# Kernel optimization log

Measured on AMD Instinct MI355X. Metric: run time of the kernel, lower is better.

Reference implementation:

```python
import jax, jax.numpy as jnp
import numpy as np

D = 768
N_HEADS = 24
WH, WW = 7, 7
N = WH * WW  # 49 tokens per window
NW = 64      # windows per image
B_ = 2048    # num_windows * batch
HEAD_DIM = D // N_HEADS
SCALE = HEAD_DIM ** -0.5


def _relative_position_index():
    # Same construction as the torch module (numpy, static).
    coords = np.stack(np.meshgrid(np.arange(WH), np.arange(WW), indexing='ij'))  # (2,Wh,Ww)
    cf = coords.reshape(2, -1)                                  # (2, N)
    rel = cf[:, :, None] - cf[:, None, :]                       # (2, N, N)
    rel = rel.transpose(1, 2, 0)                                # (N, N, 2)
    rel[:, :, 0] += WH - 1
    rel[:, :, 1] += WW - 1
    rel[:, :, 0] *= 2 * WW - 1
    return rel.sum(-1)                                          # (N, N) int

REL_IDX = jnp.asarray(_relative_position_index())


def setup_inputs() -> dict:
    key = jax.random.key(0)
    ks = jax.random.split(key, 7)
    x = jax.random.normal(ks[0], (B_, N, D), dtype=jnp.float32)
    # 0 / -100 shifted-window style mask (finite stand-in for -inf)
    mask = jnp.where(jax.random.uniform(ks[1], (NW, N, N)) < 0.1, -100.0, 0.0).astype(jnp.float32)
    qkv_w = jax.random.normal(ks[2], (D, 3 * D), dtype=jnp.float32) * (D ** -0.5)
    qkv_b = jnp.zeros((3 * D,), dtype=jnp.float32)
    proj_w = jax.random.normal(ks[3], (D, D), dtype=jnp.float32) * (D ** -0.5)
    proj_b = jnp.zeros((D,), dtype=jnp.float32)
    bias_table = jax.random.normal(ks[4], ((2 * WH - 1) * (2 * WW - 1), N_HEADS), dtype=jnp.float32) * 0.02
    return {"x": x, "mask": mask, "qkv_w": qkv_w, "qkv_b": qkv_b,
            "proj_w": proj_w, "proj_b": proj_b, "bias_table": bias_table}


def reference(x, mask, qkv_w, qkv_b, proj_w, proj_b, bias_table):
    B, n, d = x.shape
    qkv = x @ qkv_w + qkv_b                                     # (B_, n, 3d)
    q, k, v = jnp.split(qkv, 3, axis=-1)
    # (B_, n, H, hd) -> (B_, H, n, hd)
    q = q.reshape(B, n, N_HEADS, HEAD_DIM).transpose(0, 2, 1, 3)
    k = k.reshape(B, n, N_HEADS, HEAD_DIM).transpose(0, 2, 1, 3)
    v = v.reshape(B, n, N_HEADS, HEAD_DIM).transpose(0, 2, 1, 3)
    logits = jnp.einsum('bhid,bhjd->bhij', q, k) * SCALE        # (B_, H, n, n)
    rel_bias = bias_table[REL_IDX]                              # (n, n, H)
    logits = logits + rel_bias.transpose(2, 0, 1)[None]         # add (1, H, n, n)
    nW = mask.shape[0]
    logits = logits.reshape(B // nW, nW, N_HEADS, n, n) + mask[None, :, None]
    logits = logits.reshape(B, N_HEADS, n, n)
    attn = jax.nn.softmax(logits, axis=-1)
    out = jnp.einsum('bhij,bhjd->bhid', attn, v)                # (B_, H, n, hd)
    out = out.transpose(0, 2, 1, 3).reshape(B, n, d)
    return out @ proj_w + proj_b
```

## Files before the change

### kernel.cpp

```cpp
#include <hip/hip_runtime.h>

typedef __attribute__((ext_vector_type(8))) short short8;
typedef __attribute__((ext_vector_type(4))) float floatx4;
typedef __attribute__((ext_vector_type(4))) unsigned short ushort4v;

#define SCALE_F 0.17677669529663687f

__device__ __forceinline__ unsigned short f2bf(float f) {
  union { float f; unsigned u; } v; v.f = f;
  unsigned u = v.u;
  u += 0x7fffu + ((u >> 16) & 1u);
  return (unsigned short)(u >> 16);
}

__device__ __forceinline__ void gld_lds16(const void* g, void* l) {
  __builtin_amdgcn_global_load_lds((const __attribute__((address_space(1))) void*)g,
                                   (__attribute__((address_space(3))) void*)l, 16, 0, 0);
}

__global__ __launch_bounds__(256)
void cvt_bf16_k(const float* __restrict__ src, unsigned short* __restrict__ dst, long n) {
  long i = ((long)blockIdx.x * 256 + threadIdx.x) * 8;
  if (i >= n) return;
  floatx4 a0 = *(const floatx4*)(src + i);
  floatx4 a1 = *(const floatx4*)(src + i + 4);
  short8 v;
  #pragma unroll
  for (int j = 0; j < 4; ++j) { v[j] = (short)f2bf(a0[j]); v[4 + j] = (short)f2bf(a1[j]); }
  *(short8*)(dst + i) = v;
}

__global__ __launch_bounds__(256)
void transcvt_k(const float* __restrict__ W, unsigned short* __restrict__ Wt, int K, int N) {
  __shared__ float t[64][65];
  const int n0 = blockIdx.x * 64, k0 = blockIdx.y * 64;
  const int tx = threadIdx.x & 15, ty = threadIdx.x >> 4;
  #pragma unroll
  for (int r = 0; r < 4; ++r) {
    floatx4 v = *(const floatx4*)&W[(long)(k0 + ty + r * 16) * N + n0 + tx * 4];
    #pragma unroll
    for (int j = 0; j < 4; ++j) t[ty + r * 16][tx * 4 + j] = v[j];
  }
  __syncthreads();
  #pragma unroll
  for (int r = 0; r < 4; ++r) {
    ushort4v o;
    #pragma unroll
    for (int j = 0; j < 4; ++j) o[j] = f2bf(t[tx * 4 + j][ty + r * 16]);
    *(ushort4v*)&Wt[(long)(n0 + ty + r * 16) * K + k0 + tx * 4] = o;
  }
}

template<bool OUT_F32>
__global__ __launch_bounds__(512, 2)
void gemm256(const unsigned short* __restrict__ A, const unsigned short* __restrict__ Bt,
             const float* __restrict__ bias, void* __restrict__ Cp,
             int M, int N, int K, int ntN) {
  __shared__ __align__(16) unsigned short sm[2][2][256 * 64];
  (void)M;
  const int tid  = threadIdx.x;
  const int wave = tid >> 6, lane = tid & 63;
  const int quad = lane >> 4, l15 = lane & 15;
  const int wm = wave >> 2, wn = wave & 3;
  const int xorw = (l15 & 7) << 3;

  const int nwg = gridDim.x;
  const int wg  = (blockIdx.x & 7) * (nwg >> 3) + (blockIdx.x >> 3);
  const int tileN = wg % ntN, tileM = wg / ntN;
  const int NT = K >> 6;

  const int srow = tid >> 3;
  const int sg   = (tid & 7) ^ (srow & 7);
  const unsigned short* Asrc = A  + (long)(tileM * 256 + srow) * K + sg * 8;
  const unsigned short* Bsrc = Bt + (long)(tileN * 256 + srow) * K + sg * 8;

#define STG(bufi, isB, h, tt) do {                                              \
    const unsigned short* _s = (isB) ? Bsrc : Asrc;                             \
    unsigned short* _d = &sm[bufi][isB][((h) * 128 + wave * 8) * 64];           \
    gld_lds16(_s + (long)((h) * 128) * K + (tt) * 64, _d);                      \
    gld_lds16(_s + (long)((h) * 128 + 64) * K + (tt) * 64, _d + 64 * 64);       \
  } while (0)

#define RD_A(mt, kk) (*(const short8*)&sm[cur][0][(wm * 128 + (mt) * 16 + l15) * 64 + (((kk) * 32 + quad * 8) ^ xorw)])
#define RD_B(nt, kk) (*(const short8*)&sm[cur][1][(wn * 64  + (nt) * 16 + l15) * 64 + (((kk) * 32 + quad * 8) ^ xorw)])

  short8 aF[4][2], bF[4][2];
  floatx4 acc[8][4] = {};

  STG(0, 1, 0, 0);
  STG(0, 0, 0, 0);
  STG(0, 0, 1, 0);
  STG(0, 1, 1, 0);
  if (NT > 1) {
    STG(1, 1, 0, 1);
    STG(1, 0, 0, 1);
    asm volatile("s_waitcnt vmcnt(4)" ::: "memory");
  } else {
    asm volatile("s_waitcnt vmcnt(0)" ::: "memory");
  }
  __builtin_amdgcn_s_barrier();

  for (int t = 0; t < NT; ++t) {
    const int cur = t & 1;
    #pragma unroll
    for (int mt = 0; mt < 4; ++mt)
      #pragma unroll
      for (int kk = 0; kk < 2; ++kk) aF[mt][kk] = RD_A(mt, kk);
    #pragma unroll
    for (int nt = 0; nt < 2; ++nt)
      #pragma unroll
      for (int kk = 0; kk < 2; ++kk) bF[nt][kk] = RD_B(nt, kk);
    if (t + 1 < NT) STG(cur ^ 1, 0, 1, t + 1);
    __builtin_amdgcn_s_barrier();
    asm volatile("s_waitcnt lgkmcnt(0)" ::: "memory");
    __builtin_amdgcn_s_setprio(1);
    #pragma unroll
    for (int mt = 0; mt < 4; ++mt)
      #pragma unroll
      for (int nt = 0; nt < 2; ++nt)
        #pragma unroll
        for (int kk = 0; kk < 2; ++kk)
          acc[mt][nt] = __builtin_amdgcn_mfma_f32_16x16x32_bf16(aF[mt][kk], bF[nt][kk], acc[mt][nt], 0, 0, 0);
    __builtin_amdgcn_s_setprio(0);
    __builtin_amdgcn_s_barrier();

    #pragma unroll
    for (int nt = 2; nt < 4; ++nt)
      #pragma unroll
      for (int kk = 0; kk < 2; ++kk) bF[nt][kk] = RD_B(nt, kk);
    if (t + 1 < NT) STG(cur ^ 1, 1, 1, t + 1);
    __builtin_amdgcn_s_barrier();
    asm volatile("s_waitcnt lgkmcnt(0)" ::: "memory");
    __builtin_amdgcn_s_setprio(1);
    #pragma unroll
    for (int mt = 0; mt < 4; ++mt)
      #pragma unroll
      for (int nt = 2; nt < 4; ++nt)
        #pragma unroll
        for (int kk = 0; kk < 2; ++kk)
          acc[mt][nt] = __builtin_amdgcn_mfma_f32_16x16x32_bf16(aF[mt][kk], bF[nt][kk], acc[mt][nt], 0, 0, 0);
    __builtin_amdgcn_s_setprio(0);
    __builtin_amdgcn_s_barrier();

    #pragma unroll
    for (int mt = 0; mt < 4; ++mt)
      #pragma unroll
      for (int kk = 0; kk < 2; ++kk) aF[mt][kk] = RD_A(mt + 4, kk);
    if (t + 2 < NT) STG(cur, 1, 0, t + 2);
    __builtin_amdgcn_s_barrier();
    asm volatile("s_waitcnt lgkmcnt(0)" ::: "memory");
    __builtin_amdgcn_s_setprio(1);
    #pragma unroll
    for (int mt = 0; mt < 4; ++mt)
      #pragma unroll
      for (int nt = 2; nt < 4; ++nt)
        #pragma unroll
        for (int kk = 0; kk < 2; ++kk)
          acc[mt + 4][nt] = __builtin_amdgcn_mfma_f32_16x16x32_bf16(aF[mt][kk], bF[nt][kk], acc[mt + 4][nt], 0, 0, 0);
    __builtin_amdgcn_s_setprio(0);
    __builtin_amdgcn_s_barrier();

    if (t + 2 < NT) STG(cur, 0, 0, t + 2);
    __builtin_amdgcn_s_setprio(1);
    #pragma unroll
    for (int mt = 0; mt < 4; ++mt)
      #pragma unroll
      for (int nt = 0; nt < 2; ++nt)
        #pragma unroll
        for (int kk = 0; kk < 2; ++kk)
          acc[mt + 4][nt] = __builtin_amdgcn_mfma_f32_16x16x32_bf16(aF[mt][kk], bF[nt][kk], acc[mt + 4][nt], 0, 0, 0);
    __builtin_amdgcn_s_setprio(0);
    if (t + 2 < NT)      { asm volatile("s_waitcnt vmcnt(4)" ::: "memory"); }
    else if (t + 1 < NT) { asm volatile("s_waitcnt vmcnt(0)" ::: "memory"); }
    __builtin_amdgcn_s_barrier();
  }
#undef STG
#undef RD_A
#undef RD_B

  float bv[4];
  #pragma unroll
  for (int nt = 0; nt < 4; ++nt) bv[nt] = bias[tileN * 256 + wn * 64 + nt * 16 + l15];
  #pragma unroll
  for (int mt = 0; mt < 8; ++mt)
    #pragma unroll
    for (int nt = 0; nt < 4; ++nt)
      #pragma unroll
      for (int r = 0; r < 4; ++r) {
        long rg = (long)tileM * 256 + wm * 128 + mt * 16 + quad * 4 + r;
        long cg = (long)tileN * 256 + wn * 64 + nt * 16 + l15;
        float val = acc[mt][nt][r] + bv[nt];
        if (OUT_F32) ((float*)Cp)[rg * (long)N + cg] = val;
        else         ((unsigned short*)Cp)[rg * (long)N + cg] = f2bf(val);
      }
}

__global__ __launch_bounds__(256)
void attn_k(const unsigned short* __restrict__ qkv, const float* __restrict__ mask,
            const float* __restrict__ bias_table, unsigned short* __restrict__ attn_out) {
  __shared__ __align__(16) unsigned short P[4][64][72];
  const int wave = threadIdx.x >> 6, lane = threadIdx.x & 63;
  const int quad = lane >> 4, l15 = lane & 15;
  const int flat = blockIdx.x * 4 + wave;
  const int b = flat / 24, h = flat % 24;

  const unsigned short* qbase = qkv + (long)b * 49 * 2304 + h * 32;
  const unsigned short* kbase = qbase + 768;
  const unsigned short* vbase = qbase + 1536;

  short8 qF[4], kF[4];
  #pragma unroll
  for (int mt = 0; mt < 4; ++mt) {
    int m = mt * 16 + l15; int me = m < 49 ? m : 48;
    qF[mt] = *(const short8*)(qbase + (long)me * 2304 + quad * 8);
  }
  #pragma unroll
  for (int nt = 0; nt < 4; ++nt) {
    int n = nt * 16 + l15; int ne = n < 49 ? n : 48;
    kF[nt] = *(const short8*)(kbase + (long)ne * 2304 + quad * 8);
  }

  floatx4 sc[4][4] = {};
  #pragma unroll
  for (int mt = 0; mt < 4; ++mt)
    #pragma unroll
    for (int nt = 0; nt < 4; ++nt)
      sc[mt][nt] = __builtin_amdgcn_mfma_f32_16x16x32_bf16(qF[mt], kF[nt], sc[mt][nt], 0, 0, 0);

  const int w = b & 63;
  const float* mrow = mask + (long)w * 49 * 49;
  #pragma unroll
  for (int mt = 0; mt < 4; ++mt)
    #pragma unroll
    for (int r = 0; r < 4; ++r) {
      int i = mt * 16 + quad * 4 + r;
      bool iv = i < 49;
      int ri = i / 7, ci = i % 7;
      float vals[4];
      float vmax = -1e30f;
      #pragma unroll
      for (int nt = 0; nt < 4; ++nt) {
        int j = nt * 16 + l15;
        float v = -1e30f;
        if (iv && j < 49) {
          int rj = j / 7, cj = j % 7;
          int idx = (ri - rj + 6) * 13 + (ci - cj + 6);
          v = sc[mt][nt][r] * SCALE_F + bias_table[idx * 24 + h] + mrow[i * 49 + j];
        }
        vals[nt] = v;
        vmax = fmaxf(vmax, v);
      }
      #pragma unroll
      for (int d = 1; d < 16; d <<= 1) vmax = fmaxf(vmax, __shfl_xor(vmax, d));
      float sum = 0.f;
      #pragma unroll
      for (int nt = 0; nt < 4; ++nt) { float e = __expf(vals[nt] - vmax); vals[nt] = e; sum += e; }
      #pragma unroll
      for (int d = 1; d < 16; d <<= 1) sum += __shfl_xor(sum, d);
      float inv = 1.0f / sum;
      #pragma unroll
      for (int nt = 0; nt < 4; ++nt)
        P[wave][i][nt * 16 + l15] = f2bf(vals[nt] * inv);
    }
  __syncthreads();

  floatx4 o[4][2] = {};
  #pragma unroll
  for (int kt = 0; kt < 2; ++kt) {
    short8 pF[4];
    #pragma unroll
    for (int mt = 0; mt < 4; ++mt)
      pF[mt] = *(const short8*)&P[wave][mt * 16 + l15][kt * 32 + quad * 8];
    short8 vF[2];
    #pragma unroll
    for (int nt = 0; nt < 2; ++nt) {
      short8 t;
      #pragma unroll
      for (int jj = 0; jj < 8; ++jj) {
        int j = kt * 32 + quad * 8 + jj; int je = j < 49 ? j : 48;
        t[jj] = (short)vbase[(long)je * 2304 + nt * 16 + l15];
      }
      vF[nt] = t;
    }
    #pragma unroll
    for (int mt = 0; mt < 4; ++mt)
      #pragma unroll
      for (int nt = 0; nt < 2; ++nt)
        o[mt][nt] = __builtin_amdgcn_mfma_f32_16x16x32_bf16(pF[mt], vF[nt], o[mt][nt], 0, 0, 0);
  }

  unsigned short* obase = attn_out + (long)b * 49 * 768 + h * 32;
  #pragma unroll
  for (int mt = 0; mt < 4; ++mt)
    #pragma unroll
    for (int nt = 0; nt < 2; ++nt)
      #pragma unroll
      for (int r = 0; r < 4; ++r) {
        int i = mt * 16 + quad * 4 + r;
        if (i < 49) obase[(long)i * 768 + nt * 16 + l15] = f2bf(o[mt][nt][r]);
      }
}

extern "C" void kernel_launch(void* const* d_in, const int* in_sizes, int n_in,
                              void* d_out, int out_size, void* d_ws, size_t ws_size,
                              hipStream_t stream) {
  const float* x          = (const float*)d_in[0];
  const float* mask       = (const float*)d_in[1];
  const float* qkv_w      = (const float*)d_in[2];
  const float* qkv_b      = (const float*)d_in[3];
  const float* proj_w     = (const float*)d_in[4];
  const float* proj_b     = (const float*)d_in[5];
  const float* bias_table = (const float*)d_in[6];

  unsigned short* xb      = (unsigned short*)d_out;
  unsigned short* qkv_wt  = (unsigned short*)d_out + (size_t)100352 * 768;
  unsigned short* qkv     = (unsigned short*)d_ws;
  unsigned short* attn    = qkv + (size_t)100352 * 2304;
  unsigned short* proj_wt = qkv;
  float* out = (float*)d_out;

  const long nx = (long)100352 * 768;
  cvt_bf16_k<<<(nx / 8 + 255) / 256, 256, 0, stream>>>(x, xb, nx);
  transcvt_k<<<dim3(36, 12), 256, 0, stream>>>(qkv_w, qkv_wt, 768, 2304);
  gemm256<false><<<dim3(3528), 512, 0, stream>>>(xb, qkv_wt, qkv_b, qkv, 100352, 2304, 768, 9);
  attn_k<<<12288, 256, 0, stream>>>(qkv, mask, bias_table, attn);
  transcvt_k<<<dim3(12, 12), 256, 0, stream>>>(proj_w, proj_wt, 768, 768);
  gemm256<true><<<dim3(1176), 512, 0, stream>>>(attn, proj_wt, proj_b, out, 100352, 768, 768, 3);
}
```

Measured before the change: 1.278 ms.

## Write V transposed per window from QKV GEMM epilogue for vectorized attention loads

The QKV GEMM epilogue now splits its output: Q and K go to a compact 1536-wide buffer, and V is written transposed into a per-window [b][channel][64] layout. The attention kernel then reads V fragments with single 16-byte loads instead of eight scalar strided gathers. MFMA sections are also bracketed with raised wave priority. The cost is scattered 2-byte stores in the GEMM epilogue and a larger padded V buffer placed in the output region.

```diff
diff --git a/kernel.cpp b/kernel.cpp
--- a/kernel.cpp
+++ b/kernel.cpp
@@ -55,9 +55,10 @@
 __global__ __launch_bounds__(512, 2)
 void gemm256(const unsigned short* __restrict__ A, const unsigned short* __restrict__ Bt,
              const float* __restrict__ bias, void* __restrict__ Cp,
-             int M, int N, int K, int ntN) {
+             unsigned short* __restrict__ Vt, int ldC, int vSplit,
+             int N, int K, int ntN) {
   __shared__ __align__(16) unsigned short sm[2][2][256 * 64];
-  (void)M;
+  (void)N;
   const int tid  = threadIdx.x;
   const int wave = tid >> 6, lane = tid & 63;
   const int quad = lane >> 4, l15 = lane & 15;
@@ -181,51 +182,71 @@
   float bv[4];
   #pragma unroll
   for (int nt = 0; nt < 4; ++nt) bv[nt] = bias[tileN * 256 + wn * 64 + nt * 16 + l15];
-  #pragma unroll
-  for (int mt = 0; mt < 8; ++mt)
-    #pragma unroll
-    for (int nt = 0; nt < 4; ++nt)
+  const int cg0 = tileN * 256 + wn * 64;
+
+  if (cg0 >= vSplit) {
+    #pragma unroll
+    for (int mt = 0; mt < 8; ++mt)
       #pragma unroll
       for (int r = 0; r < 4; ++r) {
-        long rg = (long)tileM * 256 + wm * 128 + mt * 16 + quad * 4 + r;
-        long cg = (long)tileN * 256 + wn * 64 + nt * 16 + l15;
-        float val = acc[mt][nt][r] + bv[nt];
-        if (OUT_F32) ((float*)Cp)[rg * (long)N + cg] = val;
-        else         ((unsigned short*)Cp)[rg * (long)N + cg] = f2bf(val);
+        int rg = tileM * 256 + wm * 128 + mt * 16 + quad * 4 + r;
+        int b = rg / 49, i = rg - b * 49;
+        #pragma unroll
+        for (int nt = 0; nt < 4; ++nt) {
+          int c = cg0 + nt * 16 + l15 - vSplit;
+          Vt[((long)b * 768 + c) * 64 + i] = f2bf(acc[mt][nt][r] + bv[nt]);
+        }
       }
+  } else {
+    #pragma unroll
+    for (int mt = 0; mt < 8; ++mt)
+      #pragma unroll
+      for (int nt = 0; nt < 4; ++nt)
+        #pragma unroll
+        for (int r = 0; r < 4; ++r) {
+          long rg = (long)tileM * 256 + wm * 128 + mt * 16 + quad * 4 + r;
+          long cg = cg0 + nt * 16 + l15;
+          float val = acc[mt][nt][r] + bv[nt];
+          if (OUT_F32) ((float*)Cp)[rg * (long)ldC + cg] = val;
+          else         ((unsigned short*)Cp)[rg * (long)ldC + cg] = f2bf(val);
+        }
+  }
 }
 
 __global__ __launch_bounds__(256)
-void attn_k(const unsigned short* __restrict__ qkv, const float* __restrict__ mask,
-            const float* __restrict__ bias_table, unsigned short* __restrict__ attn_out) {
+void attn_k(const unsigned short* __restrict__ qk, const unsigned short* __restrict__ Vt,
+            const float* __restrict__ mask, const float* __restrict__ bias_table,
+            unsigned short* __restrict__ attn_out) {
   __shared__ __align__(16) unsigned short P[4][64][72];
   const int wave = threadIdx.x >> 6, lane = threadIdx.x & 63;
   const int quad = lane >> 4, l15 = lane & 15;
   const int flat = blockIdx.x * 4 + wave;
   const int b = flat / 24, h = flat % 24;
 
-  const unsigned short* qbase = qkv + (long)b * 49 * 2304 + h * 32;
+  const unsigned short* qbase = qk + (long)b * 49 * 1536 + h * 32;
   const unsigned short* kbase = qbase + 768;
-  const unsigned short* vbase = qbase + 1536;
+  const unsigned short* vtb = Vt + ((long)b * 768 + h * 32) * 64;
 
   short8 qF[4], kF[4];
   #pragma unroll
   for (int mt = 0; mt < 4; ++mt) {
     int m = mt * 16 + l15; int me = m < 49 ? m : 48;
-    qF[mt] = *(const short8*)(qbase + (long)me * 2304 + quad * 8);
+    qF[mt] = *(const short8*)(qbase + (long)me * 1536 + quad * 8);
   }
   #pragma unroll
   for (int nt = 0; nt < 4; ++nt) {
     int n = nt * 16 + l15; int ne = n < 49 ? n : 48;
-    kF[nt] = *(const short8*)(kbase + (long)ne * 2304 + quad * 8);
+    kF[nt] = *(const short8*)(kbase + (long)ne * 1536 + quad * 8);
   }
 
   floatx4 sc[4][4] = {};
+  __builtin_amdgcn_s_setprio(1);
   #pragma unroll
   for (int mt = 0; mt < 4; ++mt)
     #pragma unroll
     for (int nt = 0; nt < 4; ++nt)
       sc[mt][nt] = __builtin_amdgcn_mfma_f32_16x16x32_bf16(qF[mt], kF[nt], sc[mt][nt], 0, 0, 0);
+  __builtin_amdgcn_s_setprio(0);
 
   const int w = b & 63;
   const float* mrow = mask + (long)w * 49 * 49;
@@ -272,21 +293,24 @@
     for (int mt = 0; mt < 4; ++mt)
       pF[mt] = *(const short8*)&P[wave][mt * 16 + l15][kt * 32 + quad * 8];
     short8 vF[2];
+    const int j0 = kt * 32 + quad * 8;
     #pragma unroll
     for (int nt = 0; nt < 2; ++nt) {
-      short8 t;
-      #pragma unroll
-      for (int jj = 0; jj < 8; ++jj) {
-        int j = kt * 32 + quad * 8 + jj; int je = j < 49 ? j : 48;
-        t[jj] = (short)vbase[(long)je * 2304 + nt * 16 + l15];
+      short8 vv = short8{0, 0, 0, 0, 0, 0, 0, 0};
+      if (j0 <= 48) vv = *(const short8*)&vtb[(long)(nt * 16 + l15) * 64 + j0];
+      if (j0 == 48) {
+        #pragma unroll
+        for (int e = 1; e < 8; ++e) vv[e] = 0;
       }
-      vF[nt] = t;
+      vF[nt] = vv;
     }
+    __builtin_amdgcn_s_setprio(1);
     #pragma unroll
     for (int mt = 0; mt < 4; ++mt)
       #pragma unroll
       for (int nt = 0; nt < 2; ++nt)
         o[mt][nt] = __builtin_amdgcn_mfma_f32_16x16x32_bf16(pF[mt], vF[nt], o[mt][nt], 0, 0, 0);
+    __builtin_amdgcn_s_setprio(0);
   }
 
   unsigned short* obase = attn_out + (long)b * 49 * 768 + h * 32;
@@ -312,18 +336,21 @@
   const float* proj_b     = (const float*)d_in[5];
   const float* bias_table = (const float*)d_in[6];
 
-  unsigned short* xb      = (unsigned short*)d_out;
-  unsigned short* qkv_wt  = (unsigned short*)d_out + (size_t)100352 * 768;
-  unsigned short* qkv     = (unsigned short*)d_ws;
-  unsigned short* attn    = qkv + (size_t)100352 * 2304;
-  unsigned short* proj_wt = qkv;
+  unsigned short* qk      = (unsigned short*)d_ws;
+  unsigned short* attn    = qk + (size_t)100352 * 1536;
+  unsigned short* xb      = attn;
+  unsigned short* qkv_wt  = (unsigned short*)d_out;
+  unsigned short* Vt      = (unsigned short*)d_out + (size_t)2304 * 768;
+  unsigned short* proj_wt = qk;
   float* out = (float*)d_out;
 
   const long nx = (long)100352 * 768;
   cvt_bf16_k<<<(nx / 8 + 255) / 256, 256, 0, stream>>>(x, xb, nx);
   transcvt_k<<<dim3(36, 12), 256, 0, stream>>>(qkv_w, qkv_wt, 768, 2304);
-  gemm256<false><<<dim3(3528), 512, 0, stream>>>(xb, qkv_wt, qkv_b, qkv, 100352, 2304, 768, 9);
-  attn_k<<<12288, 256, 0, stream>>>(qkv, mask, bias_table, attn);
+  gemm256<false><<<dim3(3528), 512, 0, stream>>>(xb, qkv_wt, qkv_b, qk, Vt,
+                                                 1536, 1536, 2304, 768, 9);
+  attn_k<<<12288, 256, 0, stream>>>(qk, Vt, mask, bias_table, attn);
   transcvt_k<<<dim3(12, 12), 256, 0, stream>>>(proj_w, proj_wt, 768, 768);
-  gemm256<true><<<dim3(1176), 512, 0, stream>>>(attn, proj_wt, proj_b, out, 100352, 768, 768, 3);
-}
+  gemm256<true><<<dim3(1176), 512, 0, stream>>>(attn, proj_wt, proj_b, out, nullptr,
+                                                768, 1 << 30, 768, 768, 3);
+}
```

Result: slower. 1.421 ms (+11.2%).
